# Performance work log

Hardware: AMD Instinct MI355X
Metric: run time of the kernel (lower is better)

The kernel has to match this reference:

```python
import jax, jax.numpy as jnp
import numpy as np

N_W, N_D = 50000, 20000
E_WW, E_WD = 500000, 300000
IN, HID, OUT = 256, 128, 128


def _glorot(key, shape):
    fan_in, fan_out = shape
    s = (2.0 / (fan_in + fan_out)) ** 0.5
    return jax.random.normal(key, shape, dtype=jnp.float32) * s


def setup_inputs() -> dict:
    key = jax.random.key(0)
    ks = jax.random.split(key, 32)
    d = {}
    d['x_word'] = jax.random.normal(ks[0], (N_W, IN), dtype=jnp.float32)
    d['x_doc'] = jax.random.normal(ks[1], (N_D, IN), dtype=jnp.float32)
    # edge lists per relation (src, dst)
    d['src_ww'] = jax.random.randint(ks[2], (E_WW,), 0, N_W, dtype=jnp.int32)
    d['dst_ww'] = jax.random.randint(ks[3], (E_WW,), 0, N_W, dtype=jnp.int32)
    d['src_wd'] = jax.random.randint(ks[4], (E_WD,), 0, N_W, dtype=jnp.int32)
    d['dst_wd'] = jax.random.randint(ks[5], (E_WD,), 0, N_D, dtype=jnp.int32)
    d['src_wwr'] = jax.random.randint(ks[6], (E_WW,), 0, N_W, dtype=jnp.int32)
    d['dst_wwr'] = jax.random.randint(ks[7], (E_WW,), 0, N_W, dtype=jnp.int32)
    d['src_dwr'] = jax.random.randint(ks[8], (E_WD,), 0, N_D, dtype=jnp.int32)
    d['dst_dwr'] = jax.random.randint(ks[9], (E_WD,), 0, N_W, dtype=jnp.int32)
    # per-layer, per-relation GraphConv weights and biases
    dims = [(IN, HID), (HID, OUT)]
    i = 10
    for layer in (1, 2):
        shp = dims[layer - 1]
        for rel in ('ww', 'wd', 'wwr', 'dwr'):
            d[f'W{layer}_{rel}'] = _glorot(ks[i], shp); i += 1
            d[f'b{layer}_{rel}'] = jnp.zeros((shp[1],), jnp.float32)
    d['lin_w'] = _glorot(ks[i], (OUT, 1))
    d['lin_b'] = jnp.ones((1,), jnp.float32)
    return d


def _gconv(x_src, W, b, src, dst, n_src, n_dst):
    # DGL GraphConv, norm='both': D_dst^{-1/2} A D_src^{-1/2} X W + b
    ones = jnp.ones(src.shape[0], x_src.dtype)
    deg_o = jnp.clip(jax.ops.segment_sum(ones, src, num_segments=n_src), 1.0)
    deg_i = jnp.clip(jax.ops.segment_sum(ones, dst, num_segments=n_dst), 1.0)
    h = (x_src * jax.lax.rsqrt(deg_o)[:, None]) @ W  # weight first (in >= out)
    agg = jax.ops.segment_sum(h[src], dst, num_segments=n_dst)  # [n_dst, out]
    return agg * jax.lax.rsqrt(deg_i)[:, None] + b


def reference(x_word, x_doc,
              src_ww, dst_ww, src_wd, dst_wd, src_wwr, dst_wwr, src_dwr, dst_dwr,
              W1_ww, b1_ww, W1_wd, b1_wd, W1_wwr, b1_wwr, W1_dwr, b1_dwr,
              W2_ww, b2_ww, W2_wd, b2_wd, W2_wwr, b2_wwr, W2_dwr, b2_dwr,
              lin_w, lin_b):
    def layer(xw, xd, W_ww, b_ww, W_wd, b_wd, W_wwr, b_wwr, W_dwr, b_dwr):
        # 'word' dst: stack over 3 relations then sum == sum of contributions
        w_new = (_gconv(xw, W_ww, b_ww, src_ww, dst_ww, N_W, N_W)
                 + _gconv(xw, W_wwr, b_wwr, src_wwr, dst_wwr, N_W, N_W)
                 + _gconv(xd, W_dwr, b_dwr, src_dwr, dst_dwr, N_D, N_W))
        d_new = _gconv(xw, W_wd, b_wd, src_wd, dst_wd, N_W, N_D)
        return jax.nn.relu(w_new), jax.nn.relu(d_new)

    xw, xd = layer(x_word, x_doc, W1_ww, b1_ww, W1_wd, b1_wd, W1_wwr, b1_wwr, W1_dwr, b1_dwr)
    xw, xd = layer(xw, xd, W2_ww, b2_ww, W2_wd, b2_wd, W2_wwr, b2_wwr, W2_dwr, b2_dwr)
    out_w = jax.nn.sigmoid(xw @ lin_w + lin_b)  # [N_W, 1]
    out_d = jax.nn.sigmoid(xd @ lin_w + lin_b)  # [N_D, 1]
    return out_w, out_d
```

## Files before the change

kernel.cpp:

```cpp
#include <hip/hip_runtime.h>
#include <hip/hip_bf16.h>


#define N_W 50000
#define N_D 20000
#define E_WW 500000
#define E_WD 300000
#define NTOT 170000

#define C_WW 40
#define C_WD 48
#define C_DWR 32

#define NB_WW 196
#define NB_WD 79
#define NB_DWR 196

#define CAPB_WW 2816
#define CAPB_WD 4096
#define CAPB_DWR 1792

typedef __attribute__((ext_vector_type(8))) short short8;
typedef __attribute__((ext_vector_type(4))) float f32x4;

static __device__ __forceinline__ unsigned f2bf_u(float x) {
  unsigned u = __float_as_uint(x);
  return (u + 0x7fff + ((u >> 16) & 1)) >> 16;
}
static __device__ __forceinline__ unsigned short f2bf(float x) {
  return (unsigned short)f2bf_u(x);
}
static __device__ __forceinline__ float bf2f(unsigned short b) {
  return __uint_as_float((unsigned)b << 16);
}
static __device__ __forceinline__ void gld16(const void* g, void* l) {
  __builtin_amdgcn_global_load_lds(
      (const __attribute__((address_space(1))) void*)g,
      (__attribute__((address_space(3))) void*)l, 16, 0, 0);
}

struct Args {
  const float *x_word, *x_doc;
  const int *src_ww, *dst_ww, *src_wd, *dst_wd, *src_wwr, *dst_wwr, *src_dwr, *dst_dwr;
  const float *W1_ww, *W1_wd, *W1_wwr, *W1_dwr;
  const float *W2_ww, *W2_wd, *W2_wwr, *W2_dwr;
  const float *b1_ww, *b1_wd, *b1_wwr, *b1_dwr;
  const float *b2_ww, *b2_wd, *b2_wwr, *b2_dwr;
  const float *lin_w, *lin_b;
  float *out;
  int *dego4;
  int *cnt256;
  int *cur;
  unsigned short *csr_ww, *csr_wwr, *csr_wd, *csr_dwr;
  unsigned int *stg_ww, *stg_wwr, *stg_wd, *stg_dwr;
  unsigned short *xw_bf, *xd_bf, *h_w3, *h_d, *Bt1w, *Bt1d, *Bt2w, *Bt2d;
  unsigned short *accW1, *accD1;
};

#define BS_WW 123
#define BS_WD 74
#define BV_W 12500
#define BV_D 5000
#define BP1W 384
#define BP1D 128
#define BP2W 192
#define BP2D 64
#define BG_W 391
#define BG_D 157
#define BGR_W 6250
#define BGR_D 2500

static __device__ void dev_pass1(
    const int* __restrict__ src, const int* __restrict__ dst, int E,
    int* __restrict__ dego4, int degoOff, unsigned int* __restrict__ stage,
    int CAPB, int* __restrict__ cnt256rel, int lb, int shard,
    int* cnt, int* bas, int* scn, unsigned int* lstage) {
  const int t = threadIdx.x;
  cnt[t] = 0;
  __syncthreads();
  const int eb = lb * 4096;
  unsigned int w[16];
#pragma unroll
  for (int u = 0; u < 16; u++) {
    int e = eb + u * 256 + t;
    if (e < E) {
      int s = src[e], d = dst[e];
      w[u] = ((unsigned)s << 16) | (unsigned)d;
      atomicAdd(&cnt[d >> 8], 1);
      atomicAdd(&dego4[shard * NTOT + degoOff + s], 1);
    } else {
      w[u] = 0xFFFFFFFFu;
    }
  }
  __syncthreads();
  scn[t] = cnt[t];
  __syncthreads();
#pragma unroll
  for (int off = 1; off < 256; off <<= 1) {
    int v = (t >= off) ? scn[t - off] : 0;
    __syncthreads();
    scn[t] += v;
    __syncthreads();
  }
  bas[t] = scn[t] - cnt[t];
  scn[t] = bas[t];
  __syncthreads();
#pragma unroll
  for (int u = 0; u < 16; u++) {
    if (w[u] != 0xFFFFFFFFu) {
      int bk = (w[u] & 0xFFFFu) >> 8;
      int p = atomicAdd(&scn[bk], 1);
      lstage[p] = w[u];
    }
  }
  __syncthreads();
  int n = cnt[t];
  if (n > 0) {
    int g = atomicAdd(&cnt256rel[t], n);
    unsigned int* dp = stage + (size_t)t * CAPB + g;
    int lb2 = bas[t];
    for (int k = 0; k < n; k++)
      if (g + k < CAPB) dp[k] = lstage[lb2 + k];
  }
}

static __device__ __forceinline__ void dev_cvt(
    const float* __restrict__ x, unsigned short* __restrict__ y, int i, int n4) {
  if (i < n4) {
    float4 v = ((const float4*)x)[i];
    ushort4 u;
    u.x = f2bf(v.x); u.y = f2bf(v.y); u.z = f2bf(v.z); u.w = f2bf(v.w);
    ((ushort4*)y)[i] = u;
  }
}
static __device__ __forceinline__ void dev_packB(
    const float* __restrict__ W0, const float* __restrict__ W1,
    const float* __restrict__ W2, int kshift, int total, int i,
    unsigned short* __restrict__ out) {
  if (i >= total) return;
  int n = i >> kshift, k = i & ((1 << kshift) - 1);
  const float* W = (n < 128) ? W0 : ((n < 256) ? W1 : W2);
  out[i] = f2bf(W[(size_t)k * 128 + (n & 127)]);
}

__global__ __launch_bounds__(256) void prep1_kernel(Args a) {
  __shared__ int cnt[256], bas[256], scn[256];
  __shared__ unsigned int lstage[4096];
  int b = blockIdx.x;
  const int t = threadIdx.x;
  const int shard = blockIdx.x & 3;
  if (b < BS_WW) { dev_pass1(a.src_ww, a.dst_ww, E_WW, a.dego4, 0, a.stg_ww, CAPB_WW, a.cnt256, b, shard, cnt, bas, scn, lstage); return; }
  b -= BS_WW;
  if (b < BS_WW) { dev_pass1(a.src_wwr, a.dst_wwr, E_WW, a.dego4, 50000, a.stg_wwr, CAPB_WW, a.cnt256 + 256, b, shard, cnt, bas, scn, lstage); return; }
  b -= BS_WW;
  if (b < BS_WD) { dev_pass1(a.src_wd, a.dst_wd, E_WD, a.dego4, 100000, a.stg_wd, CAPB_WD, a.cnt256 + 512, b, shard, cnt, bas, scn, lstage); return; }
  b -= BS_WD;
  if (b < BS_WD) { dev_pass1(a.src_dwr, a.dst_dwr, E_WD, a.dego4, 150000, a.stg_dwr, CAPB_DWR, a.cnt256 + 768, b, shard, cnt, bas, scn, lstage); return; }
  b -= BS_WD;
  if (b < BV_W) { dev_cvt(a.x_word, a.xw_bf, b * 256 + t, N_W * 64); return; }
  b -= BV_W;
  if (b < BV_D) { dev_cvt(a.x_doc, a.xd_bf, b * 256 + t, N_D * 64); return; }
  b -= BV_D;
  if (b < BP1W) { dev_packB(a.W1_ww, a.W1_wwr, a.W1_wd, 8, 384 * 256, b * 256 + t, a.Bt1w); return; }
  b -= BP1W;
  if (b < BP1D) { dev_packB(a.W1_dwr, a.W1_dwr, a.W1_dwr, 8, 128 * 256, b * 256 + t, a.Bt1d); return; }
  b -= BP1D;
  if (b < BP2W) { dev_packB(a.W2_ww, a.W2_wwr, a.W2_wd, 7, 384 * 128, b * 256 + t, a.Bt2w); return; }
  b -= BP2W;
  dev_packB(a.W2_dwr, a.W2_dwr, a.W2_dwr, 7, 128 * 128, b * 256 + t, a.Bt2d);
}

static __device__ void dev_pass2(
    const unsigned int* __restrict__ stage, int CAPB, int C, int Nrel,
    const int* __restrict__ cnt256rel, int* __restrict__ curRel,
    unsigned short* __restrict__ csr, int b,
    int* cnt2, unsigned short* slice) {
  const int t = threadIdx.x;
  cnt2[t] = 0;
  __syncthreads();
  int n = cnt256rel[b];
  if (n > CAPB) n = CAPB;
  const unsigned int* sp = stage + (size_t)b * CAPB;
  for (int e = t; e < n; e += 256) {
    unsigned int w = sp[e];
    int dl = w & 0xFF;
    int s = w >> 16;
    int p = atomicAdd(&cnt2[dl], 1);
    if (p < C) slice[dl * C + p] = (unsigned short)s;
  }
  __syncthreads();
  const int words = 256 * C / 2;
  unsigned int* g32 = (unsigned int*)csr + (size_t)b * (128 * C);
  const unsigned int* s32 = (const unsigned int*)slice;
  for (int i = t; i < words; i += 256) g32[i] = s32[i];
  int node = b * 256 + t;
  if (node < Nrel) curRel[node] = cnt2[t];
}

__global__ __launch_bounds__(256) void pass2_kernel(Args a) {
  __shared__ int cnt2[256];
  __shared__ unsigned short slice[256 * 48];
  int b = blockIdx.x;
  if (b < NB_WW) { dev_pass2(a.stg_ww, CAPB_WW, C_WW, N_W, a.cnt256, a.cur, a.csr_ww, b, cnt2, slice); return; }
  b -= NB_WW;
  if (b < NB_WW) { dev_pass2(a.stg_wwr, CAPB_WW, C_WW, N_W, a.cnt256 + 256, a.cur + 50000, a.csr_wwr, b, cnt2, slice); return; }
  b -= NB_WW;
  if (b < NB_WD) { dev_pass2(a.stg_wd, CAPB_WD, C_WD, N_D, a.cnt256 + 512, a.cur + 100000, a.csr_wd, b, cnt2, slice); return; }
  b -= NB_WD;
  dev_pass2(a.stg_dwr, CAPB_DWR, C_DWR, N_W, a.cnt256 + 768, a.cur + 120000, a.csr_dwr, b, cnt2, slice);
}

template <int K>
static __device__ void dev_gemm(
    const unsigned short* __restrict__ A, int M,
    const unsigned short* __restrict__ BtSub,
    const int* __restrict__ dego,
    unsigned short* __restrict__ C, int cstride, int coloff,
    int bx, unsigned char* smem) {
  const int row0 = bx * 128;
  const int tid = threadIdx.x;
  const int lane = tid & 63;
  const int wave = tid >> 6;
  const int wr = wave >> 1;
  const int wc = wave & 1;
  const int lc = lane & 15;
  const int quad = lane >> 4;

  unsigned char* sA = smem;
  unsigned char* sB = smem + 16384;
  const int mn = tid & 127;
  const int kc0 = tid >> 7;
  const unsigned short* arow = A + (size_t)(row0 + mn) * K;
  const unsigned short* brow = BtSub + (size_t)mn * K;
  unsigned char* ldsA = sA + wave * 1024;
  unsigned char* ldsB = sB + wave * 1024;

  f32x4 acc[4][4];
#pragma unroll
  for (int p = 0; p < 4; p++)
#pragma unroll
    for (int q = 0; q < 4; q++) acc[p][q] = {0.f, 0.f, 0.f, 0.f};

  for (int k0 = 0; k0 < K; k0 += 64) {
#pragma unroll
    for (int i = 0; i < 4; i++) {
      int kk = k0 + (i * 2 + kc0) * 8;
      gld16(arow + kk, ldsA + i * 4096);
      gld16(brow + kk, ldsB + i * 4096);
    }
    __syncthreads();
#pragma unroll
    for (int s = 0; s < 2; s++) {
      const int ko = (s * 4 + quad) * 2048 + lc * 16;
      short8 av[4], bv[4];
#pragma unroll
      for (int p = 0; p < 4; p++)
        av[p] = *(const short8*)(sA + ko + (wr * 64 + p * 16) * 16);
#pragma unroll
      for (int q = 0; q < 4; q++)
        bv[q] = *(const short8*)(sB + ko + (wc * 64 + q * 16) * 16);
#pragma unroll
      for (int p = 0; p < 4; p++)
#pragma unroll
        for (int q = 0; q < 4; q++)
          acc[p][q] = __builtin_amdgcn_mfma_f32_16x16x32_bf16(
              av[p], bv[q], acc[p][q], 0, 0, 0);
    }
    __syncthreads();
  }

  const int colb = coloff + wc * 64;
#pragma unroll
  for (int p = 0; p < 4; p++) {
#pragma unroll
    for (int i = 0; i < 4; i++) {
      int r = row0 + wr * 64 + p * 16 + quad * 4 + i;
      if (r >= M) continue;
      int dg = dego[r] + dego[NTOT + r] + dego[2 * NTOT + r] + dego[3 * NTOT + r];
      float sc = rsqrtf(fmaxf((float)dg, 1.0f));
      unsigned short* cp = C + (size_t)r * cstride + colb + lc;
#pragma unroll
      for (int q = 0; q < 4; q++) cp[q * 16] = f2bf(acc[p][q][i] * sc);
    }
  }
}

__global__ __launch_bounds__(256) void gemm1_kernel(Args a) {
  __shared__ __align__(16) unsigned char smem[32768];
  int b = blockIdx.x;
  if (b < BG_W) { dev_gemm<256>(a.xw_bf, N_W, a.Bt1w,                     a.dego4,          a.h_w3, 384, 0,   b, smem); return; }
  b -= BG_W;
  if (b < BG_W) { dev_gemm<256>(a.xw_bf, N_W, a.Bt1w + (size_t)128 * 256, a.dego4 + 50000,  a.h_w3, 384, 128, b, smem); return; }
  b -= BG_W;
  if (b < BG_W) { dev_gemm<256>(a.xw_bf, N_W, a.Bt1w + (size_t)256 * 256, a.dego4 + 100000, a.h_w3, 384, 256, b, smem); return; }
  b -= BG_W;
  dev_gemm<256>(a.xd_bf, N_D, a.Bt1d, a.dego4 + 150000, a.h_d, 128, 0, b, smem);
}

__global__ __launch_bounds__(256) void gemm2_kernel(Args a) {
  __shared__ __align__(16) unsigned char smem[32768];
  int b = blockIdx.x;
  if (b < BG_W) { dev_gemm<128>(a.accW1, N_W, a.Bt2w,                     a.dego4,          a.h_w3, 384, 0,   b, smem); return; }
  b -= BG_W;
  if (b < BG_W) { dev_gemm<128>(a.accW1, N_W, a.Bt2w + (size_t)128 * 128, a.dego4 + 50000,  a.h_w3, 384, 128, b, smem); return; }
  b -= BG_W;
  if (b < BG_W) { dev_gemm<128>(a.accW1, N_W, a.Bt2w + (size_t)256 * 128, a.dego4 + 100000, a.h_w3, 384, 256, b, smem); return; }
  b -= BG_W;
  dev_gemm<128>(a.accD1, N_D, a.Bt2d, a.dego4 + 150000, a.h_d, 128, 0, b, smem);
}

static __device__ __forceinline__ float4 edge_sum32(
    const unsigned short* __restrict__ base, int stride,
    const unsigned short* __restrict__ csr, int st, int en, int lane32) {
  float4 s0 = make_float4(0.f, 0.f, 0.f, 0.f);
  float4 s1 = make_float4(0.f, 0.f, 0.f, 0.f);
  float4 s2 = make_float4(0.f, 0.f, 0.f, 0.f);
  float4 s3 = make_float4(0.f, 0.f, 0.f, 0.f);
  for (int b = st; b < en; b += 32) {
    int n = en - b; if (n > 32) n = 32;
    int t = b + lane32;
    int idx = csr[t < en ? t : en - 1];
    int j = 0;
    for (; j + 3 < n; j += 4) {
      int e0 = __shfl(idx, j, 32), e1 = __shfl(idx, j + 1, 32);
      int e2 = __shfl(idx, j + 2, 32), e3 = __shfl(idx, j + 3, 32);
      ushort4 u0 = *(const ushort4*)(base + (size_t)e0 * stride);
      ushort4 u1 = *(const ushort4*)(base + (size_t)e1 * stride);
      ushort4 u2 = *(const ushort4*)(base + (size_t)e2 * stride);
      ushort4 u3 = *(const ushort4*)(base + (size_t)e3 * stride);
      s0.x += bf2f(u0.x); s0.y += bf2f(u0.y); s0.z += bf2f(u0.z); s0.w += bf2f(u0.w);
      s1.x += bf2f(u1.x); s1.y += bf2f(u1.y); s1.z += bf2f(u1.z); s1.w += bf2f(u1.w);
      s2.x += bf2f(u2.x); s2.y += bf2f(u2.y); s2.z += bf2f(u2.z); s2.w += bf2f(u2.w);
      s3.x += bf2f(u3.x); s3.y += bf2f(u3.y); s3.z += bf2f(u3.z); s3.w += bf2f(u3.w);
    }
    for (; j < n; j++) {
      int e0 = __shfl(idx, j, 32);
      ushort4 u0 = *(const ushort4*)(base + (size_t)e0 * stride);
      s0.x += bf2f(u0.x); s0.y += bf2f(u0.y); s0.z += bf2f(u0.z); s0.w += bf2f(u0.w);
    }
  }
  return make_float4(s0.x + s1.x + s2.x + s3.x, s0.y + s1.y + s2.y + s3.y,
                     s0.z + s1.z + s2.z + s3.z, s0.w + s1.w + s2.w + s3.w);
}

template <int HEAD>
__global__ __launch_bounds__(256) void gather_kernel(Args a) {
  const int lane32 = threadIdx.x & 31;
  const int f = lane32 * 4;
  int blk = blockIdx.x;
  float v[4];
  float* outp;
  unsigned short* accp;

  if (blk < BGR_W) {
    int g = blk * 8 + (threadIdx.x >> 5);
    int c1 = a.cur[g];
    int c2 = a.cur[50000 + g];
    int c3 = a.cur[120000 + g];
    int l1 = c1 < C_WW ? c1 : C_WW;
    int l2 = c2 < C_WW ? c2 : C_WW;
    int l3 = c3 < C_DWR ? c3 : C_DWR;
    float4 s1 = edge_sum32(a.h_w3 + f, 384, a.csr_ww, g * C_WW, g * C_WW + l1, lane32);
    float4 s2 = edge_sum32(a.h_w3 + 128 + f, 384, a.csr_wwr, g * C_WW, g * C_WW + l2, lane32);
    float4 s3 = edge_sum32(a.h_d + f, 128, a.csr_dwr, g * C_DWR, g * C_DWR + l3, lane32);
    float r1 = rsqrtf(fmaxf((float)c1, 1.f));
    float r2 = rsqrtf(fmaxf((float)c2, 1.f));
    float r3 = rsqrtf(fmaxf((float)c3, 1.f));
    const float* b0 = HEAD ? a.b2_ww : a.b1_ww;
    const float* b1 = HEAD ? a.b2_wwr : a.b1_wwr;
    const float* b2 = HEAD ? a.b2_dwr : a.b1_dwr;
#pragma unroll
    for (int i = 0; i < 4; i++) {
      float bb = b0[f + i] + b1[f + i] + b2[f + i];
      v[i] = fmaxf((&s1.x)[i] * r1 + (&s2.x)[i] * r2 + (&s3.x)[i] * r3 + bb, 0.f);
    }
    outp = a.out + g;
    accp = a.accW1 + (size_t)g * 128 + f;
  } else {
    int g = (blk - BGR_W) * 8 + (threadIdx.x >> 5);
    int c1 = a.cur[100000 + g];
    int l1 = c1 < C_WD ? c1 : C_WD;
    float4 s1 = edge_sum32(a.h_w3 + 256 + f, 384, a.csr_wd, g * C_WD, g * C_WD + l1, lane32);
    float r1 = rsqrtf(fmaxf((float)c1, 1.f));
    const float* b0 = HEAD ? a.b2_wd : a.b1_wd;
#pragma unroll
    for (int i = 0; i < 4; i++)
      v[i] = fmaxf((&s1.x)[i] * r1 + b0[f + i], 0.f);
    outp = a.out + N_W + g;
    accp = a.accD1 + (size_t)g * 128 + f;
  }

  if (HEAD) {
    float4 w4 = *(const float4*)(a.lin_w + f);
    float p = v[0] * w4.x + v[1] * w4.y + v[2] * w4.z + v[3] * w4.w;
#pragma unroll
    for (int off = 16; off > 0; off >>= 1) p += __shfl_down(p, off, 32);
    if (lane32 == 0) *outp = 1.0f / (1.0f + expf(-(p + a.lin_b[0])));
  } else {
    ushort4 o;
    o.x = f2bf(v[0]); o.y = f2bf(v[1]); o.z = f2bf(v[2]); o.w = f2bf(v[3]);
    *(ushort4*)accp = o;
  }
}

extern "C" void kernel_launch(void* const* d_in, const int* in_sizes, int n_in,
                              void* d_out, int out_size, void* d_ws, size_t ws_size,
                              hipStream_t stream) {
  Args a;
  a.x_word = (const float*)d_in[0];
  a.x_doc  = (const float*)d_in[1];
  a.src_ww  = (const int*)d_in[2];
  a.dst_ww  = (const int*)d_in[3];
  a.src_wd  = (const int*)d_in[4];
  a.dst_wd  = (const int*)d_in[5];
  a.src_wwr = (const int*)d_in[6];
  a.dst_wwr = (const int*)d_in[7];
  a.src_dwr = (const int*)d_in[8];
  a.dst_dwr = (const int*)d_in[9];
  a.W1_ww  = (const float*)d_in[10]; a.b1_ww  = (const float*)d_in[11];
  a.W1_wd  = (const float*)d_in[12]; a.b1_wd  = (const float*)d_in[13];
  a.W1_wwr = (const float*)d_in[14]; a.b1_wwr = (const float*)d_in[15];
  a.W1_dwr = (const float*)d_in[16]; a.b1_dwr = (const float*)d_in[17];
  a.W2_ww  = (const float*)d_in[18]; a.b2_ww  = (const float*)d_in[19];
  a.W2_wd  = (const float*)d_in[20]; a.b2_wd  = (const float*)d_in[21];
  a.W2_wwr = (const float*)d_in[22]; a.b2_wwr = (const float*)d_in[23];
  a.W2_dwr = (const float*)d_in[24]; a.b2_dwr = (const float*)d_in[25];
  a.lin_w  = (const float*)d_in[26];
  a.lin_b  = (const float*)d_in[27];
  a.out = (float*)d_out;

  char* ws = (char*)d_ws;
  size_t off = 0;
  auto alloc = [&](size_t n4) { void* p = ws + off * 4; off += n4; return p; };
  a.dego4  = (int*)alloc((size_t)4 * NTOT);
  a.cnt256 = (int*)alloc(1024);
  const size_t zero4 = off;
  a.cur = (int*)alloc(NTOT);
  a.csr_ww  = (unsigned short*)alloc((size_t)NB_WW * 256 * C_WW / 2);
  a.csr_wwr = (unsigned short*)alloc((size_t)NB_WW * 256 * C_WW / 2);
  a.csr_wd  = (unsigned short*)alloc((size_t)NB_WD * 256 * C_WD / 2);
  a.csr_dwr = (unsigned short*)alloc((size_t)NB_DWR * 256 * C_DWR / 2);
  a.xw_bf = (unsigned short*)alloc((size_t)N_W * 256 / 2);
  a.xd_bf = (unsigned short*)alloc((size_t)N_D * 256 / 2);
  a.h_w3  = (unsigned short*)alloc((size_t)N_W * 384 / 2);
  a.h_d   = (unsigned short*)alloc((size_t)N_D * 128 / 2);
  a.Bt1w  = (unsigned short*)alloc(384 * 256 / 2);
  a.Bt1d  = (unsigned short*)alloc(128 * 256 / 2);
  a.Bt2w  = (unsigned short*)alloc(384 * 128 / 2);
  a.Bt2d  = (unsigned short*)alloc(128 * 128 / 2);
  a.accW1 = a.xw_bf;
  a.accD1 = a.xw_bf + (size_t)N_W * 128;
  unsigned int* stg = (unsigned int*)a.h_w3;
  a.stg_ww  = stg;                       stg += (size_t)NB_WW * CAPB_WW;
  a.stg_wwr = stg;                       stg += (size_t)NB_WW * CAPB_WW;
  a.stg_wd  = stg;                       stg += (size_t)NB_WD * CAPB_WD;
  a.stg_dwr = stg;
  (void)ws_size;

  hipMemsetAsync(d_ws, 0, zero4 * 4, stream);

  prep1_kernel<<<2 * BS_WW + 2 * BS_WD + BV_W + BV_D + BP1W + BP1D + BP2W + BP2D,
                 256, 0, stream>>>(a);
  pass2_kernel<<<2 * NB_WW + NB_WD + NB_DWR, 256, 0, stream>>>(a);
  gemm1_kernel<<<3 * BG_W + BG_D, 256, 0, stream>>>(a);
  gather_kernel<0><<<BGR_W + BGR_D, 256, 0, stream>>>(a);
  gemm2_kernel<<<3 * BG_W + BG_D, 256, 0, stream>>>(a);
  gather_kernel<1><<<BGR_W + BGR_D, 256, 0, stream>>>(a);
}
```

Before: 465.1 us.

## Replace global atomic out-degree counting with source-bucketed LDS histogram pass

Out-degrees are no longer counted with scattered global atomics into a 4-way sharded array during pass1. Instead, each pass1 block also bucket-sorts its edges by the high byte of the source id into per-bucket byte staging buffers, and new pass2 blocks count degrees in LDS and write precomputed rsqrt(max(deg,1)) floats. The GEMM epilogues then read one float per row instead of summing four int shards and taking rsqrt. This trades random global atomics for an extra local scan and sort plus extra staging traffic, and it relies on fixed per-bucket capacity limits that could overflow with skewed inputs.

Result: faster. 374.2 us (-19.5%).

```diff
diff --git a/kernel.cpp b/kernel.cpp
--- a/kernel.cpp
+++ b/kernel.cpp
@@ -15,10 +15,15 @@
 #define NB_WW 196
 #define NB_WD 79
 #define NB_DWR 196
-
 #define CAPB_WW 2816
 #define CAPB_WD 4096
 #define CAPB_DWR 1792
+
+#define NBS_W 196
+#define NBS_D 79
+#define CAPS_WW 2816
+#define CAPS_WD 1792
+#define CAPS_DWR 4352
 
 typedef __attribute__((ext_vector_type(8))) short short8;
 typedef __attribute__((ext_vector_type(4))) float f32x4;
@@ -48,11 +53,13 @@
   const float *b2_ww, *b2_wd, *b2_wwr, *b2_dwr;
   const float *lin_w, *lin_b;
   float *out;
-  int *dego4;
-  int *cnt256;
+  int *cnt256d;
+  int *cnt256s;
   int *cur;
+  float *degF;
   unsigned short *csr_ww, *csr_wwr, *csr_wd, *csr_dwr;
   unsigned int *stg_ww, *stg_wwr, *stg_wd, *stg_dwr;
+  unsigned char *sst_ww, *sst_wwr, *sst_wd, *sst_dwr;
   unsigned short *xw_bf, *xd_bf, *h_w3, *h_d, *Bt1w, *Bt1d, *Bt2w, *Bt2d;
   unsigned short *accW1, *accD1;
 };
@@ -70,16 +77,32 @@
 #define BGR_W 6250
 #define BGR_D 2500
 
+static __device__ __forceinline__ void lds_scan256(int* cnt, int* bas, int* scn) {
+  const int t = threadIdx.x;
+  scn[t] = cnt[t];
+  __syncthreads();
+#pragma unroll
+  for (int off = 1; off < 256; off <<= 1) {
+    int v = (t >= off) ? scn[t - off] : 0;
+    __syncthreads();
+    scn[t] += v;
+    __syncthreads();
+  }
+  bas[t] = scn[t] - cnt[t];
+  scn[t] = bas[t];
+  __syncthreads();
+}
+
 static __device__ void dev_pass1(
     const int* __restrict__ src, const int* __restrict__ dst, int E,
-    int* __restrict__ dego4, int degoOff, unsigned int* __restrict__ stage,
-    int CAPB, int* __restrict__ cnt256rel, int lb, int shard,
-    int* cnt, int* bas, int* scn, unsigned int* lstage) {
+    unsigned int* __restrict__ stageD, int CAPBD, int* __restrict__ cntD,
+    unsigned char* __restrict__ stageS, int CAPBS, int* __restrict__ cntS,
+    int lb, int* cnt, int* bas, int* scn, unsigned int* lstage) {
   const int t = threadIdx.x;
-  cnt[t] = 0;
-  __syncthreads();
   const int eb = lb * 4096;
   unsigned int w[16];
+  cnt[t] = 0;
+  __syncthreads();
 #pragma unroll
   for (int u = 0; u < 16; u++) {
     int e = eb + u * 256 + t;
@@ -87,24 +110,12 @@
       int s = src[e], d = dst[e];
       w[u] = ((unsigned)s << 16) | (unsigned)d;
       atomicAdd(&cnt[d >> 8], 1);
-      atomicAdd(&dego4[shard * NTOT + degoOff + s], 1);
     } else {
       w[u] = 0xFFFFFFFFu;
     }
   }
   __syncthreads();
-  scn[t] = cnt[t];
-  __syncthreads();
-#pragma unroll
-  for (int off = 1; off < 256; off <<= 1) {
-    int v = (t >= off) ? scn[t - off] : 0;
-    __syncthreads();
-    scn[t] += v;
-    __syncthreads();
-  }
-  bas[t] = scn[t] - cnt[t];
-  scn[t] = bas[t];
-  __syncthreads();
+  lds_scan256(cnt, bas, scn);
 #pragma unroll
   for (int u = 0; u < 16; u++) {
     if (w[u] != 0xFFFFFFFFu) {
@@ -114,13 +125,43 @@
     }
   }
   __syncthreads();
-  int n = cnt[t];
-  if (n > 0) {
-    int g = atomicAdd(&cnt256rel[t], n);
-    unsigned int* dp = stage + (size_t)t * CAPB + g;
-    int lb2 = bas[t];
-    for (int k = 0; k < n; k++)
-      if (g + k < CAPB) dp[k] = lstage[lb2 + k];
+  {
+    int n = cnt[t];
+    if (n > 0) {
+      int g = atomicAdd(&cntD[t], n);
+      unsigned int* dp = stageD + (size_t)t * CAPBD + g;
+      int lb2 = bas[t];
+      for (int k = 0; k < n; k++)
+        if (g + k < CAPBD) dp[k] = lstage[lb2 + k];
+    }
+  }
+  __syncthreads();
+  cnt[t] = 0;
+  __syncthreads();
+#pragma unroll
+  for (int u = 0; u < 16; u++)
+    if (w[u] != 0xFFFFFFFFu) atomicAdd(&cnt[w[u] >> 24], 1);
+  __syncthreads();
+  lds_scan256(cnt, bas, scn);
+  unsigned char* lbytes = (unsigned char*)lstage;
+#pragma unroll
+  for (int u = 0; u < 16; u++) {
+    if (w[u] != 0xFFFFFFFFu) {
+      int bk = w[u] >> 24;
+      int p = atomicAdd(&scn[bk], 1);
+      lbytes[p] = (unsigned char)((w[u] >> 16) & 0xFF);
+    }
+  }
+  __syncthreads();
+  {
+    int n = cnt[t];
+    if (n > 0) {
+      int g = atomicAdd(&cntS[t], n);
+      unsigned char* dp = stageS + (size_t)t * CAPBS + g;
+      int lb2 = bas[t];
+      for (int k = 0; k < n; k++)
+        if (g + k < CAPBS) dp[k] = lbytes[lb2 + k];
+    }
   }
 }
 
@@ -148,14 +189,13 @@
   __shared__ unsigned int lstage[4096];
   int b = blockIdx.x;
   const int t = threadIdx.x;
-  const int shard = blockIdx.x & 3;
-  if (b < BS_WW) { dev_pass1(a.src_ww, a.dst_ww, E_WW, a.dego4, 0, a.stg_ww, CAPB_WW, a.cnt256, b, shard, cnt, bas, scn, lstage); return; }
+  if (b < BS_WW) { dev_pass1(a.src_ww, a.dst_ww, E_WW, a.stg_ww, CAPB_WW, a.cnt256d, a.sst_ww, CAPS_WW, a.cnt256s, b, cnt, bas, scn, lstage); return; }
   b -= BS_WW;
-  if (b < BS_WW) { dev_pass1(a.src_wwr, a.dst_wwr, E_WW, a.dego4, 50000, a.stg_wwr, CAPB_WW, a.cnt256 + 256, b, shard, cnt, bas, scn, lstage); return; }
+  if (b < BS_WW) { dev_pass1(a.src_wwr, a.dst_wwr, E_WW, a.stg_wwr, CAPB_WW, a.cnt256d + 256, a.sst_wwr, CAPS_WW, a.cnt256s + 256, b, cnt, bas, scn, lstage); return; }
   b -= BS_WW;
-  if (b < BS_WD) { dev_pass1(a.src_wd, a.dst_wd, E_WD, a.dego4, 100000, a.stg_wd, CAPB_WD, a.cnt256 + 512, b, shard, cnt, bas, scn, lstage); return; }
+  if (b < BS_WD) { dev_pass1(a.src_wd, a.dst_wd, E_WD, a.stg_wd, CAPB_WD, a.cnt256d + 512, a.sst_wd, CAPS_WD, a.cnt256s + 512, b, cnt, bas, scn, lstage); return; }
   b -= BS_WD;
-  if (b < BS_WD) { dev_pass1(a.src_dwr, a.dst_dwr, E_WD, a.dego4, 150000, a.stg_dwr, CAPB_DWR, a.cnt256 + 768, b, shard, cnt, bas, scn, lstage); return; }
+  if (b < BS_WD) { dev_pass1(a.src_dwr, a.dst_dwr, E_WD, a.stg_dwr, CAPB_DWR, a.cnt256d + 768, a.sst_dwr, CAPS_DWR, a.cnt256s + 768, b, cnt, bas, scn, lstage); return; }
   b -= BS_WD;
   if (b < BV_W) { dev_cvt(a.x_word, a.xw_bf, b * 256 + t, N_W * 64); return; }
   b -= BV_W;
@@ -172,13 +212,13 @@
 
 static __device__ void dev_pass2(
     const unsigned int* __restrict__ stage, int CAPB, int C, int Nrel,
-    const int* __restrict__ cnt256rel, int* __restrict__ curRel,
+    const int* __restrict__ cntD, int* __restrict__ curRel,
     unsigned short* __restrict__ csr, int b,
     int* cnt2, unsigned short* slice) {
   const int t = threadIdx.x;
   cnt2[t] = 0;
   __syncthreads();
-  int n = cnt256rel[b];
+  int n = cntD[b];
   if (n > CAPB) n = CAPB;
   const unsigned int* sp = stage + (size_t)b * CAPB;
   for (int e = t; e < n; e += 256) {
@@ -197,24 +237,48 @@
   if (node < Nrel) curRel[node] = cnt2[t];
 }
 
+static __device__ void dev_pass2b(
+    const unsigned char* __restrict__ stage, int CAPB, int Nrel,
+    const int* __restrict__ cntS, float* __restrict__ degFRel, int b,
+    int* cnt2) {
+  const int t = threadIdx.x;
+  cnt2[t] = 0;
+  __syncthreads();
+  int n = cntS[b];
+  if (n > CAPB) n = CAPB;
+  const unsigned char* sp = stage + (size_t)b * CAPB;
+  for (int e = t; e < n; e += 256) atomicAdd(&cnt2[sp[e]], 1);
+  __syncthreads();
+  int node = b * 256 + t;
+  if (node < Nrel) degFRel[node] = rsqrtf(fmaxf((float)cnt2[t], 1.0f));
+}
+
 __global__ __launch_bounds__(256) void pass2_kernel(Args a) {
   __shared__ int cnt2[256];
   __shared__ unsigned short slice[256 * 48];
   int b = blockIdx.x;
-  if (b < NB_WW) { dev_pass2(a.stg_ww, CAPB_WW, C_WW, N_W, a.cnt256, a.cur, a.csr_ww, b, cnt2, slice); return; }
+  if (b < NB_WW) { dev_pass2(a.stg_ww, CAPB_WW, C_WW, N_W, a.cnt256d, a.cur, a.csr_ww, b, cnt2, slice); return; }
   b -= NB_WW;
-  if (b < NB_WW) { dev_pass2(a.stg_wwr, CAPB_WW, C_WW, N_W, a.cnt256 + 256, a.cur + 50000, a.csr_wwr, b, cnt2, slice); return; }
+  if (b < NB_WW) { dev_pass2(a.stg_wwr, CAPB_WW, C_WW, N_W, a.cnt256d + 256, a.cur + 50000, a.csr_wwr, b, cnt2, slice); return; }
   b -= NB_WW;
-  if (b < NB_WD) { dev_pass2(a.stg_wd, CAPB_WD, C_WD, N_D, a.cnt256 + 512, a.cur + 100000, a.csr_wd, b, cnt2, slice); return; }
+  if (b < NB_WD) { dev_pass2(a.stg_wd, CAPB_WD, C_WD, N_D, a.cnt256d + 512, a.cur + 100000, a.csr_wd, b, cnt2, slice); return; }
   b -= NB_WD;
-  dev_pass2(a.stg_dwr, CAPB_DWR, C_DWR, N_W, a.cnt256 + 768, a.cur + 120000, a.csr_dwr, b, cnt2, slice);
+  if (b < NB_DWR) { dev_pass2(a.stg_dwr, CAPB_DWR, C_DWR, N_W, a.cnt256d + 768, a.cur + 120000, a.csr_dwr, b, cnt2, slice); return; }
+  b -= NB_DWR;
+  if (b < NBS_W) { dev_pass2b(a.sst_ww, CAPS_WW, N_W, a.cnt256s, a.degF, b, cnt2); return; }
+  b -= NBS_W;
+  if (b < NBS_W) { dev_pass2b(a.sst_wwr, CAPS_WW, N_W, a.cnt256s + 256, a.degF + 50000, b, cnt2); return; }
+  b -= NBS_W;
+  if (b < NBS_W) { dev_pass2b(a.sst_wd, CAPS_WD, N_W, a.cnt256s + 512, a.degF + 100000, b, cnt2); return; }
+  b -= NBS_W;
+  dev_pass2b(a.sst_dwr, CAPS_DWR, N_D, a.cnt256s + 768, a.degF + 150000, b, cnt2);
 }
 
 template <int K>
 static __device__ void dev_gemm(
     const unsigned short* __restrict__ A, int M,
     const unsigned short* __restrict__ BtSub,
-    const int* __restrict__ dego,
+    const float* __restrict__ degF,
     unsigned short* __restrict__ C, int cstride, int coloff,
     int bx, unsigned char* smem) {
   const int row0 = bx * 128;
@@ -276,8 +340,7 @@
     for (int i = 0; i < 4; i++) {
       int r = row0 + wr * 64 + p * 16 + quad * 4 + i;
       if (r >= M) continue;
-      int dg = dego[r] + dego[NTOT + r] + dego[2 * NTOT + r] + dego[3 * NTOT + r];
-      float sc = rsqrtf(fmaxf((float)dg, 1.0f));
+      float sc = degF[r];
       unsigned short* cp = C + (size_t)r * cstride + colb + lc;
 #pragma unroll
       for (int q = 0; q < 4; q++) cp[q * 16] = f2bf(acc[p][q][i] * sc);
@@ -288,25 +351,25 @@
 __global__ __launch_bounds__(256) void gemm1_kernel(Args a) {
   __shared__ __align__(16) unsigned char smem[32768];
   int b = blockIdx.x;
-  if (b < BG_W) { dev_gemm<256>(a.xw_bf, N_W, a.Bt1w,                     a.dego4,          a.h_w3, 384, 0,   b, smem); return; }
+  if (b < BG_W) { dev_gemm<256>(a.xw_bf, N_W, a.Bt1w,                     a.degF,          a.h_w3, 384, 0,   b, smem); return; }
   b -= BG_W;
-  if (b < BG_W) { dev_gemm<256>(a.xw_bf, N_W, a.Bt1w + (size_t)128 * 256, a.dego4 + 50000,  a.h_w3, 384, 128, b, smem); return; }
+  if (b < BG_W) { dev_gemm<256>(a.xw_bf, N_W, a.Bt1w + (size_t)128 * 256, a.degF + 50000,  a.h_w3, 384, 128, b, smem); return; }
   b -= BG_W;
-  if (b < BG_W) { dev_gemm<256>(a.xw_bf, N_W, a.Bt1w + (size_t)256 * 256, a.dego4 + 100000, a.h_w3, 384, 256, b, smem); return; }
+  if (b < BG_W) { dev_gemm<256>(a.xw_bf, N_W, a.Bt1w + (size_t)256 * 256, a.degF + 100000, a.h_w3, 384, 256, b, smem); return; }
   b -= BG_W;
-  dev_gemm<256>(a.xd_bf, N_D, a.Bt1d, a.dego4 + 150000, a.h_d, 128, 0, b, smem);
+  dev_gemm<256>(a.xd_bf, N_D, a.Bt1d, a.degF + 150000, a.h_d, 128, 0, b, smem);
 }
 
 __global__ __launch_bounds__(256) void gemm2_kernel(Args a) {
   __shared__ __align__(16) unsigned char smem[32768];
   int b = blockIdx.x;
-  if (b < BG_W) { dev_gemm<128>(a.accW1, N_W, a.Bt2w,                     a.dego4,          a.h_w3, 384, 0,   b, smem); return; }
+  if (b < BG_W) { dev_gemm<128>(a.accW1, N_W, a.Bt2w,                     a.degF,          a.h_w3, 384, 0,   b, smem); return; }
   b -= BG_W;
-  if (b < BG_W) { dev_gemm<128>(a.accW1, N_W, a.Bt2w + (size_t)128 * 128, a.dego4 + 50000,  a.h_w3, 384, 128, b, smem); return; }
+  if (b < BG_W) { dev_gemm<128>(a.accW1, N_W, a.Bt2w + (size_t)128 * 128, a.degF + 50000,  a.h_w3, 384, 128, b, smem); return; }
   b -= BG_W;
-  if (b < BG_W) { dev_gemm<128>(a.accW1, N_W, a.Bt2w + (size_t)256 * 128, a.dego4 + 100000, a.h_w3, 384, 256, b, smem); return; }
+  if (b < BG_W) { dev_gemm<128>(a.accW1, N_W, a.Bt2w + (size_t)256 * 128, a.degF + 100000, a.h_w3, 384, 256, b, smem); return; }
   b -= BG_W;
-  dev_gemm<128>(a.accD1, N_D, a.Bt2d, a.dego4 + 150000, a.h_d, 128, 0, b, smem);
+  dev_gemm<128>(a.accD1, N_D, a.Bt2d, a.degF + 150000, a.h_d, 128, 0, b, smem);
 }
 
 static __device__ __forceinline__ float4 edge_sum32(
@@ -432,10 +495,11 @@
   char* ws = (char*)d_ws;
   size_t off = 0;
   auto alloc = [&](size_t n4) { void* p = ws + off * 4; off += n4; return p; };
-  a.dego4  = (int*)alloc((size_t)4 * NTOT);
-  a.cnt256 = (int*)alloc(1024);
+  a.cnt256d = (int*)alloc(1024);
+  a.cnt256s = (int*)alloc(1024);
   const size_t zero4 = off;
-  a.cur = (int*)alloc(NTOT);
+  a.cur  = (int*)alloc(NTOT);
+  a.degF = (float*)alloc(NTOT);
   a.csr_ww  = (unsigned short*)alloc((size_t)NB_WW * 256 * C_WW / 2);
   a.csr_wwr = (unsigned short*)alloc((size_t)NB_WW * 256 * C_WW / 2);
   a.csr_wd  = (unsigned short*)alloc((size_t)NB_WD * 256 * C_WD / 2);
@@ -451,17 +515,22 @@
   a.accW1 = a.xw_bf;
   a.accD1 = a.xw_bf + (size_t)N_W * 128;
   unsigned int* stg = (unsigned int*)a.h_w3;
-  a.stg_ww  = stg;                       stg += (size_t)NB_WW * CAPB_WW;
-  a.stg_wwr = stg;                       stg += (size_t)NB_WW * CAPB_WW;
-  a.stg_wd  = stg;                       stg += (size_t)NB_WD * CAPB_WD;
-  a.stg_dwr = stg;
+  a.stg_ww  = stg;  stg += (size_t)NB_WW * CAPB_WW;
+  a.stg_wwr = stg;  stg += (size_t)NB_WW * CAPB_WW;
+  a.stg_wd  = stg;  stg += (size_t)NB_WD * CAPB_WD;
+  a.stg_dwr = stg;  stg += (size_t)NB_DWR * CAPB_DWR;
+  unsigned char* sstg = (unsigned char*)stg;
+  a.sst_ww  = sstg; sstg += (size_t)NBS_W * CAPS_WW;
+  a.sst_wwr = sstg; sstg += (size_t)NBS_W * CAPS_WW;
+  a.sst_wd  = sstg; sstg += (size_t)NBS_W * CAPS_WD;
+  a.sst_dwr = sstg;
   (void)ws_size;
 
   hipMemsetAsync(d_ws, 0, zero4 * 4, stream);
 
   prep1_kernel<<<2 * BS_WW + 2 * BS_WD + BV_W + BV_D + BP1W + BP1D + BP2W + BP2D,
                  256, 0, stream>>>(a);
-  pass2_kernel<<<2 * NB_WW + NB_WD + NB_DWR, 256, 0, stream>>>(a);
+  pass2_kernel<<<2 * NB_WW + NB_WD + NB_DWR + 3 * NBS_W + NBS_D, 256, 0, stream>>>(a);
   gemm1_kernel<<<3 * BG_W + BG_D, 256, 0, stream>>>(a);
   gather_kernel<0><<<BGR_W + BGR_D, 256, 0, stream>>>(a);
   gemm2_kernel<<<3 * BG_W + BG_D, 256, 0, stream>>>(a);
```
